# Kernel tuning notes

Measured on AMD Instinct MI355X. Metric: run time of the kernel, lower is better.

The kernel has to match this reference:

```python
import jax, jax.numpy as jnp
import numpy as np

V, D, F, K, L, R, ID, B = 50000, 64, 100, 3, 256, 10, 32, 128
IDMAX = 50


def _cnn(vec, Wc, bc, Wl, bl):
    # vec: [N, L, D] -> Conv1d over L (channels=D), ReLU, max-pool over L, Linear+tanh
    x = vec.transpose(0, 2, 1)  # [N, D, L]
    pad = (K - 1) // 2
    y = jax.lax.conv_general_dilated(x, Wc, (1,), [(pad, pad)],
                                     dimension_numbers=('NCH', 'OIH', 'NCH'))
    y = jax.nn.relu(y + bc[None, :, None])  # [N, F, L]
    y = y.max(axis=2)  # [N, F]
    return jnp.tanh(y @ Wl.T + bl)  # [N, ID]


def _fm(x, v, w, b):
    lin = x @ w.T + b  # [N, 1]
    i1 = x @ v
    i2 = (x ** 2) @ (v ** 2)
    pair = jnp.sum(i1 ** 2 - i2, axis=1)
    return (lin[:, 0] + 0.5 * pair)[:, None]


def setup_inputs() -> dict:
    key = jax.random.key(0)
    ks = iter(jax.random.split(key, 40))
    nrm = lambda shape, s=0.1: jax.random.normal(next(ks), shape, jnp.float32) * s
    ri = lambda shape, hi: jax.random.randint(next(ks), shape, 0, hi, dtype=jnp.int32)
    return dict(
        user_reviews=ri((B, R, L), V), item_reviews=ri((B, R, L), V),
        uids=ri((B,), IDMAX), iids=ri((B,), IDMAX),
        user2item=ri((B, R), IDMAX), item2user=ri((B, R), IDMAX),
        rand_reviews=ri((B, L), V),
        user_emb=nrm((V, D)), item_emb=nrm((V, D)),
        cu_Wc=nrm((F, D, K)), cu_bc=jnp.zeros((F,)), cu_Wl=nrm((ID, F)), cu_bl=jnp.zeros((ID,)),
        ci_Wc=nrm((F, D, K)), ci_bc=jnp.zeros((F,)), ci_Wl=nrm((ID, F)), ci_bl=jnp.zeros((ID,)),
        t_W1=nrm((ID, 2 * R * ID)), t_b1=jnp.full((ID,), 0.1),
        t_W2=nrm((ID, ID)), t_b2=jnp.full((ID,), 0.1),
        fs_v=jnp.full((ID, 8), 0.001), fs_w=nrm((1, ID), 0.001), fs_b=jnp.zeros((1,)),
        te_emb=nrm((V, D)),
        tc_Wc=nrm((F, D, K)), tc_bc=jnp.zeros((F,)), tc_Wl=nrm((ID, F)), tc_bl=jnp.zeros((ID,)),
        ft_v=jnp.full((ID, 8), 0.001), ft_w=nrm((1, ID), 0.001), ft_b=jnp.zeros((1,)),
    )


def reference(user_reviews, item_reviews, uids, iids, user2item, item2user, rand_reviews,
              user_emb, item_emb, cu_Wc, cu_bc, cu_Wl, cu_bl, ci_Wc, ci_bc, ci_Wl, ci_bl,
              t_W1, t_b1, t_W2, t_b2, fs_v, fs_w, fs_b,
              te_emb, tc_Wc, tc_bc, tc_Wl, tc_bl, ft_v, ft_w, ft_b):
    Bn = user_reviews.shape[0]
    ur = user_reviews.reshape(Bn * R, L)
    ir = item_reviews.reshape(Bn * R, L)
    # SourceNet
    ul = _cnn(user_emb[ur], cu_Wc, cu_bc, cu_Wl, cu_bl).reshape(Bn, R * ID)
    il = _cnn(item_emb[ir], ci_Wc, ci_bc, ci_Wl, ci_bl).reshape(Bn, R * ID)
    cat = jnp.concatenate([ul, il], axis=1)  # [B, 2*R*ID]
    h = jnp.tanh(cat @ t_W1.T + t_b1)
    src = jnp.tanh(h @ t_W2.T + t_b2)  # dropout in eval mode = identity
    _src_pred = _fm(jax.lax.stop_gradient(src), fs_v, fs_w, fs_b)  # computed, unused in output
    # Vectorized replacement of the per-sample membership/gather loop
    mu = user2item == iids[:, None]  # [B, R]
    mi = item2user == uids[:, None]  # [B, R]
    gu = user_reviews[jnp.arange(Bn), jnp.argmax(mu, axis=1)]  # first match
    gi = item_reviews[jnp.arange(Bn), jnp.argmax(mi, axis=1)]
    reviews = jnp.where(mu.any(1)[:, None], gu,
                        jnp.where(mi.any(1)[:, None], gi, rand_reviews))  # [B, L]
    # TargetNet
    tl = _cnn(te_emb[reviews], tc_Wc, tc_bc, tc_Wl, tc_bl)
    _tgt_pred = _fm(tl, ft_v, ft_w, ft_b)  # computed, unused in output
    return src, tl
```

## Files before the change

### kernel.cpp

```cpp
#include <hip/hip_runtime.h>
#include <hip/hip_bf16.h>


#define C_V 50000
#define C_D 64
#define C_F 100
#define C_K 3
#define C_L 256
#define C_R 10
#define C_ID 32
#define C_B 128

typedef unsigned int u32;
typedef unsigned short u16;
typedef __attribute__((ext_vector_type(8))) short bf16x8;
typedef __attribute__((ext_vector_type(4))) float f32x4;

__device__ __forceinline__ float bf2f(u16 h) { union {u32 u; float f;} v; v.u = ((u32)h) << 16; return v.f; }
__device__ __forceinline__ u16 f2bf(float f) {
    union {float f; u32 u;} v; v.f = f;
    u32 u = v.u;
    return (u16)((u + 0x7fffu + ((u >> 16) & 1u)) >> 16);
}
__device__ __forceinline__ float ldf(const void* p, int idx, int isf) {
    return isf ? ((const float*)p)[idx] : bf2f(((const u16*)p)[idx]);
}
__device__ __forceinline__ void stf(void* p, int idx, float v, int isf) {
    if (isf) ((float*)p)[idx] = v; else ((u16*)p)[idx] = f2bf(v);
}
__device__ __forceinline__ int detect_isf(const u32* __restrict__ ue, int lane) {
    u32 w = ue[lane];
    u32 e = (w >> 7) & 0xFFu;
    int hit = (e >= 0x70u && e <= 0x7Fu);
    unsigned long long m = __ballot(hit);
    return (__popcll(m) >= 32) ? 0 : 1;
}
__device__ __forceinline__ void gl_lds16(const void* g, void* l) {
    __builtin_amdgcn_global_load_lds(
        (const __attribute__((address_space(1))) void*)g,
        (__attribute__((address_space(3))) void*)l, 16, 0, 0);
}
__device__ __forceinline__ bf16x8 dec8(u32 w0, u32 w1) {
    union { short s[8]; bf16x8 v; } u;
    #pragma unroll
    for (int j = 0; j < 4; ++j) {
        int v0 = ((int)(w0 << (24 - 8 * j))) >> 24;
        int v1 = ((int)(w1 << (24 - 8 * j))) >> 24;
        union {float f; u32 b;} a; a.f = (float)v0;
        union {float f; u32 b;} b; b.f = (float)v1;
        u.s[j]     = (short)(a.b >> 16);
        u.s[4 + j] = (short)(b.b >> 16);
    }
    return u.v;
}

__global__ __launch_bounds__(256) void prep_quant(
    const void* __restrict__ user_emb, const void* __restrict__ item_emb,
    const void* __restrict__ te_emb, signed char* __restrict__ qtab)
{
    int gid = blockIdx.x * 256 + threadIdx.x;
    int isf = detect_isf((const u32*)user_emb, threadIdx.x & 63);
    if (gid >= 600000) return;
    int base = gid * 16;
    int set  = base / (C_V * C_D);
    int off  = base % (C_V * C_D);
    const void* src = (set == 0) ? user_emb : (set == 1) ? item_emb : te_emb;
    signed char q[16];
    #pragma unroll
    for (int j = 0; j < 16; ++j) {
        float x = ldf(src, off + j, isf);
        float r = fminf(fmaxf(rintf(x * 128.f), -127.f), 127.f);
        q[j] = (signed char)(int)r;
    }
    *reinterpret_cast<uint4*>(qtab + base) = *reinterpret_cast<const uint4*>(q);
}

__global__ __launch_bounds__(256) void prep_bfrags(
    const void* __restrict__ cu_Wc, const void* __restrict__ ci_Wc,
    const void* __restrict__ tc_Wc, const u32* __restrict__ ue,
    u16* __restrict__ wsB)
{
    int tid = threadIdx.x;
    int isf = detect_isf(ue, tid & 63);
    int id = blockIdx.x * 256 + tid;
    if (id >= 3 * 6 * 7 * 64) return;
    int s    = id / 2688;
    int rem  = id % 2688;
    int c    = rem / 448;
    int rem2 = rem % 448;
    int nt   = rem2 / 64;
    int lane = rem2 % 64;
    int f    = nt * 16 + (lane & 15);
    int quad = lane >> 4;
    const void* W = (s == 0) ? cu_Wc : (s == 1) ? ci_Wc : tc_Wc;
    u16 out[8];
    #pragma unroll
    for (int j = 0; j < 8; ++j) {
        int kdim = c * 32 + quad * 8 + j;
        int tap = kdim >> 6, d = kdim & 63;
        float v = (f < C_F) ? ldf(W, (f * C_D + d) * C_K + tap, isf) * (1.f / 128.f) : 0.f;
        out[j] = f2bf(v);
    }
    *reinterpret_cast<uint4*>(wsB + id * 8) = *reinterpret_cast<const uint4*>(out);
}

__global__ __launch_bounds__(256, 4) void cnn_mfma(
    const int* __restrict__ user_reviews, const int* __restrict__ item_reviews,
    const int* __restrict__ uids, const int* __restrict__ iids,
    const int* __restrict__ user2item, const int* __restrict__ item2user,
    const int* __restrict__ rand_reviews,
    const signed char* __restrict__ qtab, const u32* __restrict__ ue,
    const void* __restrict__ cu_bc, const void* __restrict__ cu_Wl, const void* __restrict__ cu_bl,
    const void* __restrict__ ci_bc, const void* __restrict__ ci_Wl, const void* __restrict__ ci_bl,
    const void* __restrict__ tc_bc, const void* __restrict__ tc_Wl, const void* __restrict__ tc_bl,
    const u16* __restrict__ wsB,
    float* __restrict__ ws_cat, void* __restrict__ d_out)
{
    __shared__ __align__(16) char embS[258 * 64];
    __shared__ float poolS[C_F * 4];
    __shared__ float partS[C_ID * 8];

    const int tid = threadIdx.x;
    const int idx = (blockIdx.x & 7) * 336 + (blockIdx.x >> 3);
    const int lane = tid & 63, wave = tid >> 6;
    const int isf = detect_isf(ue, lane);

    const int* toks;
    int set;
    const void *bc, *Wl, *bl;

    if (idx < C_B * C_R) {
        toks = user_reviews + idx * C_L;
        set = 0; bc = cu_bc; Wl = cu_Wl; bl = cu_bl;
    } else if (idx < 2 * C_B * C_R) {
        int j = idx - C_B * C_R;
        toks = item_reviews + j * C_L;
        set = 1; bc = ci_bc; Wl = ci_Wl; bl = ci_bl;
    } else {
        int b = idx - 2 * C_B * C_R;
        const int* t_ = rand_reviews + b * C_L;
        int iid = iids[b];
        int uid = uids[b];
        int fu = -1, fi = -1;
        for (int r = C_R - 1; r >= 0; --r) {
            if (user2item[b * C_R + r] == iid) fu = r;
            if (item2user[b * C_R + r] == uid) fi = r;
        }
        if (fu >= 0)      t_ = user_reviews + (b * C_R + fu) * C_L;
        else if (fi >= 0) t_ = item_reviews + (b * C_R + fi) * C_L;
        toks = t_;
        set = 2; bc = tc_bc; Wl = tc_Wl; bl = tc_bl;
    }

    if (tid < 16)            ((u32*)embS)[tid] = 0u;
    else if (tid < 32)       ((u32*)embS)[257 * 16 + (tid - 16)] = 0u;

    {
        int tok64 = toks[wave * 64 + lane];
        const signed char* qt = qtab + (size_t)set * C_V * C_D;
        #pragma unroll
        for (int i = 0; i < 4; ++i) {
            int sub = lane >> 2;
            int token = __shfl(tok64, i * 16 + sub);
            int row_lds = wave * 64 + i * 16 + sub + 1;
            int schunk = (lane & 3) ^ (row_lds & 3);
            const void* g = qt + (size_t)token * C_D + schunk * 16;
            void* ldsbase = embS + (size_t)(wave * 64 + i * 16 + 1) * 64;
            gl_lds16(g, ldsbase);
        }
    }
    __syncthreads();

    const int quad = lane >> 4, mcol = lane & 15;
    const int mbase = wave * 64;
    const u16* BfG = wsB + set * 21504;

    {
        f32x4 acc[4][4];
        #pragma unroll
        for (int mt = 0; mt < 4; ++mt)
            #pragma unroll
            for (int nt = 0; nt < 4; ++nt) acc[mt][nt] = (f32x4){0.f,0.f,0.f,0.f};
        #pragma unroll
        for (int c = 0; c < 6; ++c) {
            const int tap = c >> 1, dh = c & 1;
            const int g8 = dh * 4 + quad;
            bf16x8 bfr[4];
            #pragma unroll
            for (int nt = 0; nt < 4; ++nt)
                bfr[nt] = *reinterpret_cast<const bf16x8*>(BfG + ((c * 7 + nt) * 64 + lane) * 8);
            bf16x8 afr[4];
            #pragma unroll
            for (int mt = 0; mt < 4; ++mt) {
                int row = mbase + mt * 16 + mcol + tap;
                const u32* p = (const u32*)(embS + row * 64 +
                                            (((g8 >> 1) ^ (row & 3)) * 16) + (g8 & 1) * 8);
                afr[mt] = dec8(p[0], p[1]);
            }
            #pragma unroll
            for (int mt = 0; mt < 4; ++mt)
                #pragma unroll
                for (int nt = 0; nt < 4; ++nt)
                    acc[mt][nt] = __builtin_amdgcn_mfma_f32_16x16x32_bf16(
                        afr[mt], bfr[nt], acc[mt][nt], 0, 0, 0);
        }
        #pragma unroll
        for (int nt = 0; nt < 4; ++nt) {
            float mv = -1e30f;
            #pragma unroll
            for (int mt = 0; mt < 4; ++mt)
                mv = fmaxf(mv, fmaxf(fmaxf(acc[mt][nt].x, acc[mt][nt].y),
                                     fmaxf(acc[mt][nt].z, acc[mt][nt].w)));
            mv = fmaxf(mv, __shfl_xor(mv, 16));
            mv = fmaxf(mv, __shfl_xor(mv, 32));
            if (quad == 0) poolS[(nt * 16 + mcol) * 4 + wave] = mv;
        }
    }
    {
        f32x4 acc[4][3];
        #pragma unroll
        for (int mt = 0; mt < 4; ++mt)
            #pragma unroll
            for (int nt = 0; nt < 3; ++nt) acc[mt][nt] = (f32x4){0.f,0.f,0.f,0.f};
        #pragma unroll
        for (int c = 0; c < 6; ++c) {
            const int tap = c >> 1, dh = c & 1;
            const int g8 = dh * 4 + quad;
            bf16x8 bfr[3];
            #pragma unroll
            for (int nt = 0; nt < 3; ++nt)
                bfr[nt] = *reinterpret_cast<const bf16x8*>(BfG + ((c * 7 + 4 + nt) * 64 + lane) * 8);
            bf16x8 afr[4];
            #pragma unroll
            for (int mt = 0; mt < 4; ++mt) {
                int row = mbase + mt * 16 + mcol + tap;
                const u32* p = (const u32*)(embS + row * 64 +
                                            (((g8 >> 1) ^ (row & 3)) * 16) + (g8 & 1) * 8);
                afr[mt] = dec8(p[0], p[1]);
            }
            #pragma unroll
            for (int mt = 0; mt < 4; ++mt)
                #pragma unroll
                for (int nt = 0; nt < 3; ++nt)
                    acc[mt][nt] = __builtin_amdgcn_mfma_f32_16x16x32_bf16(
                        afr[mt], bfr[nt], acc[mt][nt], 0, 0, 0);
        }
        #pragma unroll
        for (int nt = 0; nt < 3; ++nt) {
            float mv = -1e30f;
            #pragma unroll
            for (int mt = 0; mt < 4; ++mt)
                mv = fmaxf(mv, fmaxf(fmaxf(acc[mt][nt].x, acc[mt][nt].y),
                                     fmaxf(acc[mt][nt].z, acc[mt][nt].w)));
            mv = fmaxf(mv, __shfl_xor(mv, 16));
            mv = fmaxf(mv, __shfl_xor(mv, 32));
            int f = (4 + nt) * 16 + mcol;
            if (quad == 0 && f < C_F) poolS[f * 4 + wave] = mv;
        }
    }
    __syncthreads();

    if (tid < C_F) {
        float m4 = fmaxf(fmaxf(poolS[tid * 4 + 0], poolS[tid * 4 + 1]),
                         fmaxf(poolS[tid * 4 + 2], poolS[tid * 4 + 3]));
        poolS[tid * 4] = fmaxf(m4 + ldf(bc, tid, isf), 0.f);
    }
    __syncthreads();

    {
        int o = tid >> 3, seg = tid & 7;
        int f0 = (seg < 4) ? seg * 13 : 52 + (seg - 4) * 12;
        int cnt = (seg < 4) ? 13 : 12;
        float acc = 0.f;
        for (int q = 0; q < cnt; ++q) {
            int f = f0 + q;
            acc += poolS[f * 4] * ldf(Wl, o * C_F + f, isf);
        }
        partS[o * 8 + seg] = acc;
    }
    __syncthreads();
    if (tid < C_ID) {
        float s = ldf(bl, tid, isf);
        #pragma unroll
        for (int q = 0; q < 8; ++q) s += partS[tid * 8 + q];
        float v = tanhf(s);
        if (idx < C_B * C_R) {
            int b = idx / C_R, r = idx % C_R;
            ws_cat[b * 640 + r * C_ID + tid] = v;
        } else if (idx < 2 * C_B * C_R) {
            int j = idx - C_B * C_R;
            int b = j / C_R, r = j % C_R;
            ws_cat[b * 640 + 320 + r * C_ID + tid] = v;
        } else {
            int b = idx - 2 * C_B * C_R;
            stf(d_out, C_B * C_ID + b * C_ID + tid, v, isf);
        }
    }
}

__global__ __launch_bounds__(256) void head_kernel(
    const float* __restrict__ ws_cat,
    const void* __restrict__ W1, const void* __restrict__ b1,
    const void* __restrict__ W2, const void* __restrict__ b2,
    const u32* __restrict__ ue, void* __restrict__ d_out)
{
    __shared__ float part[C_ID][8];
    __shared__ float h_s[C_ID];
    int b = blockIdx.x;
    int tid = threadIdx.x;
    int isf = detect_isf(ue, tid & 63);
    int o = tid >> 3, seg = tid & 7;
    const float* cat = ws_cat + b * 640;
    float acc = 0.f;
    int j0 = seg * 80;
    for (int j = j0; j < j0 + 80; ++j) acc += cat[j] * ldf(W1, o * 640 + j, isf);
    part[o][seg] = acc;
    __syncthreads();
    if (tid < C_ID) {
        float s = ldf(b1, tid, isf);
        #pragma unroll
        for (int q = 0; q < 8; ++q) s += part[tid][q];
        h_s[tid] = tanhf(s);
    }
    __syncthreads();
    if (tid < C_ID) {
        float s = ldf(b2, tid, isf);
        #pragma unroll
        for (int i = 0; i < C_ID; ++i) s += h_s[i] * ldf(W2, tid * C_ID + i, isf);
        stf(d_out, b * C_ID + tid, tanhf(s), isf);
    }
}

extern "C" void kernel_launch(void* const* d_in, const int* in_sizes, int n_in,
                              void* d_out, int out_size, void* d_ws, size_t ws_size,
                              hipStream_t stream)
{
    const int* user_reviews = (const int*)d_in[0];
    const int* item_reviews = (const int*)d_in[1];
    const int* uids         = (const int*)d_in[2];
    const int* iids         = (const int*)d_in[3];
    const int* user2item    = (const int*)d_in[4];
    const int* item2user    = (const int*)d_in[5];
    const int* rand_reviews = (const int*)d_in[6];
    const void* user_emb = d_in[7];
    const void* item_emb = d_in[8];
    const void* cu_Wc = d_in[9];
    const void* cu_bc = d_in[10];
    const void* cu_Wl = d_in[11];
    const void* cu_bl = d_in[12];
    const void* ci_Wc = d_in[13];
    const void* ci_bc = d_in[14];
    const void* ci_Wl = d_in[15];
    const void* ci_bl = d_in[16];
    const void* t_W1  = d_in[17];
    const void* t_b1  = d_in[18];
    const void* t_W2  = d_in[19];
    const void* t_b2  = d_in[20];
    const void* te_emb = d_in[24];
    const void* tc_Wc  = d_in[25];
    const void* tc_bc  = d_in[26];
    const void* tc_Wl  = d_in[27];
    const void* tc_bl  = d_in[28];

    u16*         ws_B   = (u16*)d_ws;
    signed char* ws_q   = (signed char*)((char*)d_ws + 129536);
    float*       ws_cat = (float*)((char*)d_ws + 129536 + 9600000);

    prep_quant<<<2344, 256, 0, stream>>>(user_emb, item_emb, te_emb, ws_q);

    prep_bfrags<<<32, 256, 0, stream>>>(cu_Wc, ci_Wc, tc_Wc,
                                        (const u32*)user_emb, ws_B);

    cnn_mfma<<<2 * C_B * C_R + C_B, 256, 0, stream>>>(
        user_reviews, item_reviews, uids, iids, user2item, item2user, rand_reviews,
        ws_q, (const u32*)user_emb,
        cu_bc, cu_Wl, cu_bl, ci_bc, ci_Wl, ci_bl, tc_bc, tc_Wl, tc_bl,
        ws_B, ws_cat, d_out);

    head_kernel<<<C_B, 256, 0, stream>>>(ws_cat, t_W1, t_b1, t_W2, t_b2,
                                         (const u32*)user_emb, d_out);
}
```

Baseline: 211.3 us.

## Decode int8 embeddings to bf16 once at LDS staging instead of per fragment

```diff
diff --git a/kernel.cpp b/kernel.cpp
--- a/kernel.cpp
+++ b/kernel.cpp
@@ -35,23 +35,9 @@
     unsigned long long m = __ballot(hit);
     return (__popcll(m) >= 32) ? 0 : 1;
 }
-__device__ __forceinline__ void gl_lds16(const void* g, void* l) {
-    __builtin_amdgcn_global_load_lds(
-        (const __attribute__((address_space(1))) void*)g,
-        (__attribute__((address_space(3))) void*)l, 16, 0, 0);
-}
-__device__ __forceinline__ bf16x8 dec8(u32 w0, u32 w1) {
-    union { short s[8]; bf16x8 v; } u;
-    #pragma unroll
-    for (int j = 0; j < 4; ++j) {
-        int v0 = ((int)(w0 << (24 - 8 * j))) >> 24;
-        int v1 = ((int)(w1 << (24 - 8 * j))) >> 24;
-        union {float f; u32 b;} a; a.f = (float)v0;
-        union {float f; u32 b;} b; b.f = (float)v1;
-        u.s[j]     = (short)(a.b >> 16);
-        u.s[4 + j] = (short)(b.b >> 16);
-    }
-    return u.v;
+__device__ __forceinline__ u32 pack2(float a, float b) {
+    union {float f; u32 u;} ua, ub; ua.f = a; ub.f = b;
+    return (ua.u >> 16) | (ub.u & 0xFFFF0000u);
 }
 
 __global__ __launch_bounds__(256) void prep_quant(
@@ -116,9 +102,10 @@
     const u16* __restrict__ wsB,
     float* __restrict__ ws_cat, void* __restrict__ d_out)
 {
-    __shared__ __align__(16) char embS[258 * 64];
-    __shared__ float poolS[C_F * 4];
-    __shared__ float partS[C_ID * 8];
+    __shared__ __align__(16) char smem[258 * 128 + 1600];
+    u16*   embS  = (u16*)smem;
+    float* poolS = (float*)(smem + 258 * 128);
+    float* partS = (float*)smem;
 
     const int tid = threadIdx.x;
     const int idx = (blockIdx.x & 7) * 336 + (blockIdx.x >> 3);
@@ -152,21 +139,36 @@
         set = 2; bc = tc_bc; Wl = tc_Wl; bl = tc_bl;
     }
 
-    if (tid < 16)            ((u32*)embS)[tid] = 0u;
-    else if (tid < 32)       ((u32*)embS)[257 * 16 + (tid - 16)] = 0u;
+    if (tid < 32)            ((u32*)embS)[tid] = 0u;
+    else if (tid < 64)       ((u32*)embS)[257 * 32 + (tid - 32)] = 0u;
 
     {
-        int tok64 = toks[wave * 64 + lane];
+        int token = toks[tid];
         const signed char* qt = qtab + (size_t)set * C_V * C_D;
-        #pragma unroll
-        for (int i = 0; i < 4; ++i) {
-            int sub = lane >> 2;
-            int token = __shfl(tok64, i * 16 + sub);
-            int row_lds = wave * 64 + i * 16 + sub + 1;
-            int schunk = (lane & 3) ^ (row_lds & 3);
-            const void* g = qt + (size_t)token * C_D + schunk * 16;
-            void* ldsbase = embS + (size_t)(wave * 64 + i * 16 + 1) * 64;
-            gl_lds16(g, ldsbase);
+        const uint4* src = reinterpret_cast<const uint4*>(qt + (size_t)token * C_D);
+        u32 w[16];
+        #pragma unroll
+        for (int h = 0; h < 4; ++h) {
+            uint4 v = src[h];
+            w[h * 4 + 0] = v.x; w[h * 4 + 1] = v.y;
+            w[h * 4 + 2] = v.z; w[h * 4 + 3] = v.w;
+        }
+        int rw = (tid + 1) & 7;
+        u16* dst = embS + (size_t)(tid + 1) * 64;
+        #pragma unroll
+        for (int c8 = 0; c8 < 8; ++c8) {
+            u32 out[4];
+            #pragma unroll
+            for (int pr = 0; pr < 4; ++pr) {
+                int k0 = pr * 2, k1 = pr * 2 + 1;
+                u32 ws0 = w[c8 * 2 + (k0 >> 2)];
+                u32 ws1 = w[c8 * 2 + (k1 >> 2)];
+                int b0 = ((int)(ws0 << (24 - 8 * (k0 & 3)))) >> 24;
+                int b1 = ((int)(ws1 << (24 - 8 * (k1 & 3)))) >> 24;
+                out[pr] = pack2((float)b0, (float)b1);
+            }
+            uint4 st = {out[0], out[1], out[2], out[3]};
+            *reinterpret_cast<uint4*>(dst + ((c8 ^ rw) * 8)) = st;
         }
     }
     __syncthreads();
@@ -184,7 +186,7 @@
         #pragma unroll
         for (int c = 0; c < 6; ++c) {
             const int tap = c >> 1, dh = c & 1;
-            const int g8 = dh * 4 + quad;
+            const int schunk = (dh * 4 + quad) ^ ((mcol + tap) & 7);
             bf16x8 bfr[4];
             #pragma unroll
             for (int nt = 0; nt < 4; ++nt)
@@ -193,9 +195,7 @@
             #pragma unroll
             for (int mt = 0; mt < 4; ++mt) {
                 int row = mbase + mt * 16 + mcol + tap;
-                const u32* p = (const u32*)(embS + row * 64 +
-                                            (((g8 >> 1) ^ (row & 3)) * 16) + (g8 & 1) * 8);
-                afr[mt] = dec8(p[0], p[1]);
+                afr[mt] = *reinterpret_cast<const bf16x8*>(embS + row * 64 + schunk * 8);
             }
             #pragma unroll
             for (int mt = 0; mt < 4; ++mt)
@@ -225,7 +225,7 @@
         #pragma unroll
         for (int c = 0; c < 6; ++c) {
             const int tap = c >> 1, dh = c & 1;
-            const int g8 = dh * 4 + quad;
+            const int schunk = (dh * 4 + quad) ^ ((mcol + tap) & 7);
             bf16x8 bfr[3];
             #pragma unroll
             for (int nt = 0; nt < 3; ++nt)
@@ -234,9 +234,7 @@
             #pragma unroll
             for (int mt = 0; mt < 4; ++mt) {
                 int row = mbase + mt * 16 + mcol + tap;
-                const u32* p = (const u32*)(embS + row * 64 +
-                                            (((g8 >> 1) ^ (row & 3)) * 16) + (g8 & 1) * 8);
-                afr[mt] = dec8(p[0], p[1]);
+                afr[mt] = *reinterpret_cast<const bf16x8*>(embS + row * 64 + schunk * 8);
             }
             #pragma unroll
             for (int mt = 0; mt < 4; ++mt)
```

Result: no change. 211.0 us (-0.2%).
